# Optimization experiments

Hardware: AMD Instinct MI355X
Metric: run time of the kernel (lower is better)

Reference implementation:

```python
import jax, jax.numpy as jnp
import numpy as np

C, H, W = 3, 1280, 720
BS = 20           # block size
SF = 4            # scale factor
NH, NW = H // BS, W // BS
L = NH * NW                        # 2304 blocks


def conv2d(x, w, b, stride=1):
    y = jax.lax.conv_general_dilated(
        x, w, (stride, stride), 'VALID',
        dimension_numbers=('NCHW', 'OIHW', 'NCHW'))
    return y + b[None, :, None, None]


def edge_pad1(x):
    # replicate padding=1 (padding_mode='replicate')
    return jnp.pad(x, ((0, 0), (0, 0), (1, 1), (1, 1)), mode='edge')


def zero_pad1(x):
    return jnp.pad(x, ((0, 0), (0, 0), (1, 1), (1, 1)))


def maxpool2(x):
    return jax.lax.reduce_window(x, -jnp.inf, jax.lax.max,
                                 (1, 1, 2, 2), (1, 1, 2, 2), 'VALID')


def pixel_shuffle(x, r):
    n, crr, h, w = x.shape
    c = crr // (r * r)
    x = x.reshape(n, c, r, r, h, w)
    x = x.transpose(0, 1, 4, 2, 5, 3)  # n c h r w r
    return x.reshape(n, c, h * r, w * r)


def setup_inputs() -> dict:
    key = jax.random.key(0)
    ks = jax.random.split(key, 9)

    def winit(k, shape):
        # matches torch init: std = sqrt(2 / (out_ch * kh * kw))
        std = np.sqrt(2.0 / (shape[0] * shape[2] * shape[3]))
        return jax.random.normal(k, shape, jnp.float32) * std

    return {
        'input': jax.random.uniform(ks[0], (1, C, H, W), jnp.float32),
        # gate CNN
        'w1': winit(ks[1], (16, C, 3, 3)), 'b1': jnp.zeros((16,), jnp.float32),
        'w2': winit(ks[2], (8, 16, 3, 3)), 'b2': jnp.zeros((8,), jnp.float32),
        'w3': winit(ks[3], (1, 8, BS // 4, BS // 4)), 'b3': jnp.zeros((1,), jnp.float32),
        # light expert: 3 -> 48 conv + pixel_shuffle(4)
        'wl': winit(ks[4], (C * SF * SF, C, 3, 3)), 'bl': jnp.zeros((C * SF * SF,), jnp.float32),
        # complex expert: 3 -> 32 -> 32 -> 48 + pixel_shuffle(4)
        'wc1': winit(ks[5], (32, C, 3, 3)), 'bc1': jnp.zeros((32,), jnp.float32),
        'wc2': winit(ks[6], (32, 32, 3, 3)), 'bc2': jnp.zeros((32,), jnp.float32),
        'wc3': winit(ks[7], (C * SF * SF, 32, 3, 3)), 'bc3': jnp.zeros((C * SF * SF,), jnp.float32),
    }


def _forward(input, w1, b1, w2, b2, w3, b3, wl, bl, wc1, bc1, wc2, bc2, wc3, bc3):
    # ---- gate CNN ----
    x = maxpool2(jnp.tanh(conv2d(edge_pad1(input), w1, b1)))          # [1,16,H/2,W/2]
    x = maxpool2(conv2d(edge_pad1(x), w2, b2))                        # [1,8,H/4,W/4]
    x = conv2d(x, w3, b3, stride=BS // 4)                             # [1,1,NH,NW]
    class_vector = jax.nn.sigmoid(x.reshape(-1))                      # [L]

    # ---- unfold into non-overlapping blocks (torch.nn.Unfold order) ----
    blocks = input.reshape(C, NH, BS, NW, BS).transpose(1, 3, 0, 2, 4)
    blocks = blocks.reshape(L, C, BS, BS)                             # [L,3,20,20]

    # ---- both experts on all blocks, combine by binary mask ----
    # light expert, clamp to [0,0.6] then +0.4
    light = pixel_shuffle(conv2d(zero_pad1(blocks), wl, bl), SF)
    light = jnp.clip(light, 0.0, 0.6) + 0.4
    # complex expert, clamp to [0,1]
    h1 = jax.nn.relu(conv2d(zero_pad1(blocks), wc1, bc1))
    h2 = jax.nn.relu(conv2d(zero_pad1(h1), wc2, bc2))
    comp = pixel_shuffle(conv2d(zero_pad1(h2), wc3, bc3), SF)
    comp = jnp.clip(comp, 0.0, 1.0)

    mask = class_vector > 1.0   # faithful to source (sigmoid => always False)
    out_blocks = jnp.where(mask[:, None, None, None], comp, light)    # [L,3,80,80]

    # ---- fold blocks back into the upscaled image ----
    out = out_blocks.reshape(NH, NW, C, BS * SF, BS * SF)
    out = out.transpose(2, 0, 3, 1, 4).reshape(1, C, H * SF, W * SF)  # [1,3,5120,2880]
    return out, class_vector


def reference(input, w1, b1, w2, b2, w3, b3, wl, bl, wc1, bc1, wc2, bc2, wc3, bc3):
    return _forward(input, w1, b1, w2, b2, w3, b3, wl, bl,
                    wc1, bc1, wc2, bc2, wc3, bc3)
```

## Files before the change

### kernel.cpp

```cpp
#include <hip/hip_runtime.h>
#include <math.h>

#define CC 3
#define HH 1280
#define WW 720
#define BSZ 20
#define NHB 64
#define NWB 36
#define NBLK (NHB*NWB)
#define OUT_IMG (3*5120*2880)

__global__ __launch_bounds__(256) void light_kernel(
    const float* __restrict__ inp,
    const float* __restrict__ wl,
    const float* __restrict__ bl,
    float* __restrict__ out) {
  __shared__ __align__(16) float in_s[3][22][24];
  __shared__ float w_s[48*27 + 48];
  const int l  = blockIdx.x;
  const int bi = l / NWB, bj = l % NWB;
  const int tid = threadIdx.x;

  for (int i = tid; i < 3*22*24; i += 256) ((float*)in_s)[i] = 0.0f;
  for (int i = tid; i < 48*27; i += 256) w_s[i] = wl[i];
  if (tid < 48) w_s[48*27 + tid] = bl[tid];
  __syncthreads();
  for (int i = tid; i < 300; i += 256) {
    int x4 = i % 5; int r = (i / 5) % 20; int c = i / 100;
    const float4 v = *(const float4*)&inp[(c*HH + bi*BSZ + r)*WW + bj*BSZ + 4*x4];
    float* dst = &in_s[c][r+1][1 + 4*x4];
    dst[0] = v.x; dst[1] = v.y; dst[2] = v.z; dst[3] = v.w;
  }
  __syncthreads();

  const int row0 = bi * 80, col0 = bj * 80;
  for (int pair = tid; pair < 960; pair += 256) {
    int oc = pair % 48;
    int h  = pair / 48;
    float wr[27];
    #pragma unroll
    for (int j = 0; j < 27; ++j) wr[j] = w_s[oc*27 + j];
    float acc[20];
    float bias = w_s[48*27 + oc];
    #pragma unroll
    for (int w = 0; w < 20; ++w) acc[w] = bias;

    #pragma unroll
    for (int ic = 0; ic < 3; ++ic)
      #pragma unroll
      for (int ky = 0; ky < 3; ++ky) {
        const float* row = &in_s[ic][h + ky][0];
        float r[24];
        #pragma unroll
        for (int j = 0; j < 6; ++j) {
          float4 v = ((const float4*)row)[j];
          r[j*4+0] = v.x; r[j*4+1] = v.y; r[j*4+2] = v.z; r[j*4+3] = v.w;
        }
        float w0 = wr[ic*9 + ky*3 + 0];
        float w1 = wr[ic*9 + ky*3 + 1];
        float w2 = wr[ic*9 + ky*3 + 2];
        #pragma unroll
        for (int w = 0; w < 20; ++w)
          acc[w] += r[w]*w0 + r[w+1]*w1 + r[w+2]*w2;
      }

    int c  = oc >> 4;
    int r1 = (oc >> 2) & 3;
    int r2 = oc & 3;
    int gy = row0 + h*4 + r1;
    int base = (c*5120 + gy)*2880 + col0 + r2;
    #pragma unroll
    for (int w = 0; w < 20; ++w) {
      float v = fminf(fmaxf(acc[w], 0.0f), 0.6f) + 0.4f;
      out[base + w*4] = v;
    }
  }
}

__global__ __launch_bounds__(256) void gate_fused(
    const float* __restrict__ inp,
    const float* __restrict__ w1,
    const float* __restrict__ b1,
    const float* __restrict__ w2,
    const float* __restrict__ b2,
    const float* __restrict__ w3,
    const float* __restrict__ b3,
    float* __restrict__ cv) {
  __shared__ float ins[3][26][28];
  __shared__ float w1s[16*27];
  __shared__ float b1s[16];
  __shared__ float w2s[8*16*9];
  __shared__ float b2s[8];
  __shared__ float w3s[200];
  __shared__ float b3s;
  __shared__ float x1s[16][12][13];
  __shared__ float red[256];

  const int tid = threadIdx.x;
  const int l  = blockIdx.x;
  const int oy = l / NWB, ox = l % NWB;

  for (int i = tid; i < 16*27; i += 256) w1s[i] = w1[i];
  for (int i = tid; i < 8*16*9; i += 256) w2s[i] = w2[i];
  for (int i = tid; i < 200; i += 256) w3s[i] = w3[i];
  if (tid < 16) b1s[tid] = b1[tid];
  if (tid < 8)  b2s[tid] = b2[tid];
  if (tid == 0) b3s = b3[0];

  for (int i = tid; i < 3*26*28; i += 256) {
    int b = i % 28; int a = (i / 28) % 26; int ic = i / (26*28);
    int gy = 20*oy - 3 + a; gy = gy < 0 ? 0 : (gy > HH-1 ? HH-1 : gy);
    int gx = 20*ox - 3 + b; gx = gx < 0 ? 0 : (gx > WW-1 ? WW-1 : gx);
    ins[ic][a][b] = inp[(ic*HH + gy)*WW + gx];
  }
  __syncthreads();

  for (int v = tid; v < 16*12*12; v += 256) {
    int oc = v / 144; int rem = v - oc*144; int ly = rem / 12; int lx = rem - ly*12;
    int y1 = 10*oy - 1 + ly; y1 = y1 < 0 ? 0 : (y1 > 639 ? 639 : y1);
    int x1 = 10*ox - 1 + lx; x1 = x1 < 0 ? 0 : (x1 > 359 ? 359 : x1);
    int ry = 2*y1 + 2 - 20*oy;
    int rx = 2*x1 + 2 - 20*ox;
    float patch[3][4][4];
    #pragma unroll
    for (int ic = 0; ic < 3; ++ic)
      #pragma unroll
      for (int d = 0; d < 4; ++d)
        #pragma unroll
        for (int e = 0; e < 4; ++e)
          patch[ic][d][e] = ins[ic][ry + d][rx + e];
    float m = -1e30f;
    #pragma unroll
    for (int sy = 0; sy < 2; ++sy)
      #pragma unroll
      for (int sx = 0; sx < 2; ++sx) {
        float acc = b1s[oc];
        #pragma unroll
        for (int ic = 0; ic < 3; ++ic)
          #pragma unroll
          for (int ky = 0; ky < 3; ++ky)
            #pragma unroll
            for (int kx = 0; kx < 3; ++kx)
              acc += patch[ic][sy+ky][sx+kx] * w1s[(oc*3+ic)*9 + ky*3 + kx];
        m = fmaxf(m, acc);
      }
    x1s[oc][ly][lx] = tanhf(m);
  }
  __syncthreads();

  float prod = 0.0f;
  if (tid < 200) {
    int oc2 = tid / 25; int rem = tid - oc2*25; int j = rem / 5; int i5 = rem - j*5;
    float a00 = b2s[oc2], a01 = a00, a10 = a00, a11 = a00;
    for (int ic = 0; ic < 16; ++ic) {
      float p[4][4];
      #pragma unroll
      for (int d = 0; d < 4; ++d)
        #pragma unroll
        for (int e = 0; e < 4; ++e)
          p[d][e] = x1s[ic][2*j + d][2*i5 + e];
      #pragma unroll
      for (int ky = 0; ky < 3; ++ky)
        #pragma unroll
        for (int kx = 0; kx < 3; ++kx) {
          float wv = w2s[((oc2*16 + ic)*3 + ky)*3 + kx];
          a00 += p[ky  ][kx  ]*wv;
          a01 += p[ky  ][kx+1]*wv;
          a10 += p[ky+1][kx  ]*wv;
          a11 += p[ky+1][kx+1]*wv;
        }
    }
    float x2 = fmaxf(fmaxf(a00, a01), fmaxf(a10, a11));
    prod = x2 * w3s[tid];
  }
  red[tid] = prod;
  __syncthreads();

  if (tid < 64) {
    float s = red[tid] + red[tid+64] + red[tid+128] + red[tid+192];
    #pragma unroll
    for (int off = 32; off > 0; off >>= 1) s += __shfl_down(s, off);
    if (tid == 0)
      cv[l] = 1.0f / (1.0f + expf(-(s + b3s)));
  }
}

extern "C" void kernel_launch(void* const* d_in, const int* in_sizes, int n_in,
                              void* d_out, int out_size, void* d_ws, size_t ws_size,
                              hipStream_t stream) {
  const float* inp = (const float*)d_in[0];
  const float* w1  = (const float*)d_in[1];
  const float* b1  = (const float*)d_in[2];
  const float* w2  = (const float*)d_in[3];
  const float* b2  = (const float*)d_in[4];
  const float* w3  = (const float*)d_in[5];
  const float* b3  = (const float*)d_in[6];
  const float* wl  = (const float*)d_in[7];
  const float* bl  = (const float*)d_in[8];

  float* out = (float*)d_out;

  hipLaunchKernelGGL(light_kernel, dim3(NBLK), dim3(256), 0, stream, inp, wl, bl, out);
  hipLaunchKernelGGL(gate_fused, dim3(NBLK), dim3(256), 0, stream,
                     inp, w1, b1, w2, b2, w3, b3, out + OUT_IMG);
}
```

Before: 300.4 us.

## Merge light and gate kernels into one launch and stage output through shared slab

The two kernels become a single launch in which odd blocks run the gate network and even blocks run the light expert, sharing a union of their shared-memory layouts. The light expert now writes each 5-row slab of results into shared memory and stores it to global memory as coalesced float4 rows, replacing the old strided scalar stores. Gate-side shared loads are widened to float2, and the x1s pitch becomes 14 so those loads stay aligned. The intent is to remove launch overhead, overlap the compute-heavy gate blocks with the store-bound light blocks, and make the large output write coalesced, at the cost of larger shared memory per block and extra barriers.

```diff
diff --git a/kernel.cpp b/kernel.cpp
--- a/kernel.cpp
+++ b/kernel.cpp
@@ -10,74 +10,107 @@
 #define NBLK (NHB*NWB)
 #define OUT_IMG (3*5120*2880)
 
-__global__ __launch_bounds__(256) void light_kernel(
+#define SLAB_PITCH 84
+#define SLAB_ROWS  60
+
+union __align__(16) SMem {
+  struct {
+    float in_s[3][22][24];
+    float w_s[48*27 + 48];
+    float slab[SLAB_ROWS][SLAB_PITCH];
+  } L;
+  struct {
+    float ins[3][26][28];
+    float w1s[16*27];
+    float b1s[16];
+    float w2s[8*16*9];
+    float b2s[8];
+    float w3s[200];
+    float x1s[16][12][14];
+    float red[256];
+    float b3s;
+  } G;
+};
+
+__device__ __forceinline__ void light_body(
+    SMem& sm, int l,
     const float* __restrict__ inp,
     const float* __restrict__ wl,
     const float* __restrict__ bl,
     float* __restrict__ out) {
-  __shared__ __align__(16) float in_s[3][22][24];
-  __shared__ float w_s[48*27 + 48];
-  const int l  = blockIdx.x;
   const int bi = l / NWB, bj = l % NWB;
   const int tid = threadIdx.x;
-
-  for (int i = tid; i < 3*22*24; i += 256) ((float*)in_s)[i] = 0.0f;
+  float* w_s = sm.L.w_s;
+
+  for (int i = tid; i < 3*22*24; i += 256) ((float*)sm.L.in_s)[i] = 0.0f;
   for (int i = tid; i < 48*27; i += 256) w_s[i] = wl[i];
   if (tid < 48) w_s[48*27 + tid] = bl[tid];
   __syncthreads();
   for (int i = tid; i < 300; i += 256) {
     int x4 = i % 5; int r = (i / 5) % 20; int c = i / 100;
     const float4 v = *(const float4*)&inp[(c*HH + bi*BSZ + r)*WW + bj*BSZ + 4*x4];
-    float* dst = &in_s[c][r+1][1 + 4*x4];
+    float* dst = &sm.L.in_s[c][r+1][1 + 4*x4];
     dst[0] = v.x; dst[1] = v.y; dst[2] = v.z; dst[3] = v.w;
   }
   __syncthreads();
 
   const int row0 = bi * 80, col0 = bj * 80;
-  for (int pair = tid; pair < 960; pair += 256) {
-    int oc = pair % 48;
-    int h  = pair / 48;
-    float wr[27];
-    #pragma unroll
-    for (int j = 0; j < 27; ++j) wr[j] = w_s[oc*27 + j];
-    float acc[20];
-    float bias = w_s[48*27 + oc];
-    #pragma unroll
-    for (int w = 0; w < 20; ++w) acc[w] = bias;
-
-    #pragma unroll
-    for (int ic = 0; ic < 3; ++ic)
-      #pragma unroll
-      for (int ky = 0; ky < 3; ++ky) {
-        const float* row = &in_s[ic][h + ky][0];
-        float r[24];
+
+  for (int slab = 0; slab < 4; ++slab) {
+    if (tid < 240) {
+      const int oc = tid % 48;
+      const int hl = tid / 48;
+      const int h  = slab*5 + hl;
+      float wr[27];
+      #pragma unroll
+      for (int j = 0; j < 27; ++j) wr[j] = w_s[oc*27 + j];
+      float acc[20];
+      const float bias = w_s[48*27 + oc];
+      #pragma unroll
+      for (int w = 0; w < 20; ++w) acc[w] = bias;
+
+      #pragma unroll
+      for (int ic = 0; ic < 3; ++ic)
         #pragma unroll
-        for (int j = 0; j < 6; ++j) {
-          float4 v = ((const float4*)row)[j];
-          r[j*4+0] = v.x; r[j*4+1] = v.y; r[j*4+2] = v.z; r[j*4+3] = v.w;
+        for (int ky = 0; ky < 3; ++ky) {
+          const float* row = &sm.L.in_s[ic][h + ky][0];
+          float r[24];
+          #pragma unroll
+          for (int j = 0; j < 6; ++j) {
+            float4 v = ((const float4*)row)[j];
+            r[j*4+0] = v.x; r[j*4+1] = v.y; r[j*4+2] = v.z; r[j*4+3] = v.w;
+          }
+          const float w0 = wr[ic*9 + ky*3 + 0];
+          const float w1 = wr[ic*9 + ky*3 + 1];
+          const float w2 = wr[ic*9 + ky*3 + 2];
+          #pragma unroll
+          for (int w = 0; w < 20; ++w)
+            acc[w] += r[w]*w0 + r[w+1]*w1 + r[w+2]*w2;
         }
-        float w0 = wr[ic*9 + ky*3 + 0];
-        float w1 = wr[ic*9 + ky*3 + 1];
-        float w2 = wr[ic*9 + ky*3 + 2];
-        #pragma unroll
-        for (int w = 0; w < 20; ++w)
-          acc[w] += r[w]*w0 + r[w+1]*w1 + r[w+2]*w2;
-      }
-
-    int c  = oc >> 4;
-    int r1 = (oc >> 2) & 3;
-    int r2 = oc & 3;
-    int gy = row0 + h*4 + r1;
-    int base = (c*5120 + gy)*2880 + col0 + r2;
-    #pragma unroll
-    for (int w = 0; w < 20; ++w) {
-      float v = fminf(fmaxf(acc[w], 0.0f), 0.6f) + 0.4f;
-      out[base + w*4] = v;
+
+      const int c  = oc >> 4;
+      const int r1 = (oc >> 2) & 3;
+      const int r2 = oc & 3;
+      float* dst = &sm.L.slab[c*20 + hl*4 + r1][r2];
+      #pragma unroll
+      for (int w = 0; w < 20; ++w)
+        dst[4*w] = fminf(fmaxf(acc[w], 0.0f), 0.6f) + 0.4f;
     }
-  }
-}
-
-__global__ __launch_bounds__(256) void gate_fused(
+    __syncthreads();
+
+    for (int i = tid; i < SLAB_ROWS*20; i += 256) {
+      const int rrow = i / 20, cb = i % 20;
+      const int c = rrow / 20, lr = rrow % 20;
+      const float4 v = *(const float4*)&sm.L.slab[rrow][4*cb];
+      const int gy = row0 + slab*20 + lr;
+      *(float4*)&out[(c*5120 + gy)*2880 + col0 + 4*cb] = v;
+    }
+    __syncthreads();
+  }
+}
+
+__device__ __forceinline__ void gate_body(
+    SMem& sm, int l,
     const float* __restrict__ inp,
     const float* __restrict__ w1,
     const float* __restrict__ b1,
@@ -86,32 +119,21 @@
     const float* __restrict__ w3,
     const float* __restrict__ b3,
     float* __restrict__ cv) {
-  __shared__ float ins[3][26][28];
-  __shared__ float w1s[16*27];
-  __shared__ float b1s[16];
-  __shared__ float w2s[8*16*9];
-  __shared__ float b2s[8];
-  __shared__ float w3s[200];
-  __shared__ float b3s;
-  __shared__ float x1s[16][12][13];
-  __shared__ float red[256];
-
   const int tid = threadIdx.x;
-  const int l  = blockIdx.x;
   const int oy = l / NWB, ox = l % NWB;
 
-  for (int i = tid; i < 16*27; i += 256) w1s[i] = w1[i];
-  for (int i = tid; i < 8*16*9; i += 256) w2s[i] = w2[i];
-  for (int i = tid; i < 200; i += 256) w3s[i] = w3[i];
-  if (tid < 16) b1s[tid] = b1[tid];
-  if (tid < 8)  b2s[tid] = b2[tid];
-  if (tid == 0) b3s = b3[0];
+  for (int i = tid; i < 16*27; i += 256) sm.G.w1s[i] = w1[i];
+  for (int i = tid; i < 8*16*9; i += 256) sm.G.w2s[i] = w2[i];
+  for (int i = tid; i < 200; i += 256) sm.G.w3s[i] = w3[i];
+  if (tid < 16) sm.G.b1s[tid] = b1[tid];
+  if (tid < 8)  sm.G.b2s[tid] = b2[tid];
+  if (tid == 0) sm.G.b3s = b3[0];
 
   for (int i = tid; i < 3*26*28; i += 256) {
     int b = i % 28; int a = (i / 28) % 26; int ic = i / (26*28);
     int gy = 20*oy - 3 + a; gy = gy < 0 ? 0 : (gy > HH-1 ? HH-1 : gy);
     int gx = 20*ox - 3 + b; gx = gx < 0 ? 0 : (gx > WW-1 ? WW-1 : gx);
-    ins[ic][a][b] = inp[(ic*HH + gy)*WW + gx];
+    sm.G.ins[ic][a][b] = inp[(ic*HH + gy)*WW + gx];
   }
   __syncthreads();
 
@@ -125,45 +147,48 @@
     #pragma unroll
     for (int ic = 0; ic < 3; ++ic)
       #pragma unroll
-      for (int d = 0; d < 4; ++d)
-        #pragma unroll
-        for (int e = 0; e < 4; ++e)
-          patch[ic][d][e] = ins[ic][ry + d][rx + e];
+      for (int d = 0; d < 4; ++d) {
+        const float2 pa = *(const float2*)&sm.G.ins[ic][ry + d][rx];
+        const float2 pb = *(const float2*)&sm.G.ins[ic][ry + d][rx + 2];
+        patch[ic][d][0] = pa.x; patch[ic][d][1] = pa.y;
+        patch[ic][d][2] = pb.x; patch[ic][d][3] = pb.y;
+      }
     float m = -1e30f;
     #pragma unroll
     for (int sy = 0; sy < 2; ++sy)
       #pragma unroll
       for (int sx = 0; sx < 2; ++sx) {
-        float acc = b1s[oc];
+        float acc = sm.G.b1s[oc];
         #pragma unroll
         for (int ic = 0; ic < 3; ++ic)
           #pragma unroll
           for (int ky = 0; ky < 3; ++ky)
             #pragma unroll
             for (int kx = 0; kx < 3; ++kx)
-              acc += patch[ic][sy+ky][sx+kx] * w1s[(oc*3+ic)*9 + ky*3 + kx];
+              acc += patch[ic][sy+ky][sx+kx] * sm.G.w1s[(oc*3+ic)*9 + ky*3 + kx];
         m = fmaxf(m, acc);
       }
-    x1s[oc][ly][lx] = tanhf(m);
+    sm.G.x1s[oc][ly][lx] = tanhf(m);
   }
   __syncthreads();
 
   float prod = 0.0f;
   if (tid < 200) {
     int oc2 = tid / 25; int rem = tid - oc2*25; int j = rem / 5; int i5 = rem - j*5;
-    float a00 = b2s[oc2], a01 = a00, a10 = a00, a11 = a00;
+    float a00 = sm.G.b2s[oc2], a01 = a00, a10 = a00, a11 = a00;
     for (int ic = 0; ic < 16; ++ic) {
       float p[4][4];
       #pragma unroll
-      for (int d = 0; d < 4; ++d)
-        #pragma unroll
-        for (int e = 0; e < 4; ++e)
-          p[d][e] = x1s[ic][2*j + d][2*i5 + e];
+      for (int d = 0; d < 4; ++d) {
+        const float2 pa = *(const float2*)&sm.G.x1s[ic][2*j + d][2*i5];
+        const float2 pb = *(const float2*)&sm.G.x1s[ic][2*j + d][2*i5 + 2];
+        p[d][0] = pa.x; p[d][1] = pa.y; p[d][2] = pb.x; p[d][3] = pb.y;
+      }
       #pragma unroll
       for (int ky = 0; ky < 3; ++ky)
         #pragma unroll
         for (int kx = 0; kx < 3; ++kx) {
-          float wv = w2s[((oc2*16 + ic)*3 + ky)*3 + kx];
+          float wv = sm.G.w2s[((oc2*16 + ic)*3 + ky)*3 + kx];
           a00 += p[ky  ][kx  ]*wv;
           a01 += p[ky  ][kx+1]*wv;
           a10 += p[ky+1][kx  ]*wv;
@@ -171,18 +196,37 @@
         }
     }
     float x2 = fmaxf(fmaxf(a00, a01), fmaxf(a10, a11));
-    prod = x2 * w3s[tid];
-  }
-  red[tid] = prod;
+    prod = x2 * sm.G.w3s[tid];
+  }
+  sm.G.red[tid] = prod;
   __syncthreads();
 
   if (tid < 64) {
-    float s = red[tid] + red[tid+64] + red[tid+128] + red[tid+192];
+    float s = sm.G.red[tid] + sm.G.red[tid+64] + sm.G.red[tid+128] + sm.G.red[tid+192];
     #pragma unroll
     for (int off = 32; off > 0; off >>= 1) s += __shfl_down(s, off);
     if (tid == 0)
-      cv[l] = 1.0f / (1.0f + expf(-(s + b3s)));
-  }
+      cv[l] = 1.0f / (1.0f + expf(-(s + sm.G.b3s)));
+  }
+}
+
+__global__ __launch_bounds__(256) void fused_kernel(
+    const float* __restrict__ inp,
+    const float* __restrict__ w1,
+    const float* __restrict__ b1,
+    const float* __restrict__ w2,
+    const float* __restrict__ b2,
+    const float* __restrict__ w3,
+    const float* __restrict__ b3,
+    const float* __restrict__ wl,
+    const float* __restrict__ bl,
+    float* __restrict__ out) {
+  __shared__ SMem sm;
+  const int bid = blockIdx.x;
+  if (bid & 1)
+    gate_body(sm, bid >> 1, inp, w1, b1, w2, b2, w3, b3, out + OUT_IMG);
+  else
+    light_body(sm, bid >> 1, inp, wl, bl, out);
 }
 
 extern "C" void kernel_launch(void* const* d_in, const int* in_sizes, int n_in,
@@ -200,7 +244,6 @@
 
   float* out = (float*)d_out;
 
-  hipLaunchKernelGGL(light_kernel, dim3(NBLK), dim3(256), 0, stream, inp, wl, bl, out);
-  hipLaunchKernelGGL(gate_fused, dim3(NBLK), dim3(256), 0, stream,
-                     inp, w1, b1, w2, b2, w3, b3, out + OUT_IMG);
-}
+  hipLaunchKernelGGL(fused_kernel, dim3(2*NBLK), dim3(256), 0, stream,
+                     inp, w1, b1, w2, b2, w3, b3, wl, bl, out);
+}
```

Result: faster. 270.5 us (-9.9%).
